# Kernel tuning notes

Measured on AMD Instinct MI355X. Metric: run time of the kernel, lower is better.

## Reference

```python
import jax, jax.numpy as jnp
import numpy as np

EPS = 1e-6
LN_EPS = 1e-5

def _ln(x, g, b):
    m = x.mean(-1, keepdims=True)
    v = x.var(-1, keepdims=True)
    return (x - m) / jnp.sqrt(v + LN_EPS) * g + b

def _gelu(x):
    return jax.nn.gelu(x, approximate=False)  # torch nn.GELU default (erf)

def _compress(x, W1, b1, g1, B1, W2, b2, g2, B2, W3, b3):
    h = _ln(_gelu(x @ W1 + b1), g1, B1)
    h = _ln(_gelu(h @ W2 + b2), g2, B2)
    return h @ W3 + b3

def _decompress(x, W1, b1, g1, B1, W2, b2, g2, B2, W3, b3):
    h = _ln(_gelu(x @ W1 + b1), g1, B1)
    h = _ln(_gelu(h @ W2 + b2), g2, B2)
    return h @ W3 + b3

def setup_inputs() -> dict:
    key = jax.random.key(0)
    ks = jax.random.split(key, 12)
    B, D, C, N = 1024, 1024, 256, 100000
    s = 0.02
    return {
        "query": jax.random.normal(ks[0], (B, D), jnp.float32),
        "keys_c": jax.random.normal(ks[1], (N, C), jnp.float32),
        "values_c": jax.random.normal(ks[2], (N, C), jnp.float32),
        "cW1": jax.random.normal(ks[3], (D, D // 2), jnp.float32) * s,
        "cb1": jnp.zeros((D // 2,), jnp.float32),
        "cg1": jnp.ones((D // 2,), jnp.float32),
        "cB1": jnp.zeros((D // 2,), jnp.float32),
        "cW2": jax.random.normal(ks[4], (D // 2, D // 4), jnp.float32) * s,
        "cb2": jnp.zeros((D // 4,), jnp.float32),
        "cg2": jnp.ones((D // 4,), jnp.float32),
        "cB2": jnp.zeros((D // 4,), jnp.float32),
        "cW3": jax.random.normal(ks[5], (D // 4, C), jnp.float32) * s,
        "cb3": jnp.zeros((C,), jnp.float32),
        "dW1": jax.random.normal(ks[6], (C, D // 4), jnp.float32) * s,
        "db1": jnp.zeros((D // 4,), jnp.float32),
        "dg1": jnp.ones((D // 4,), jnp.float32),
        "dB1": jnp.zeros((D // 4,), jnp.float32),
        "dW2": jax.random.normal(ks[7], (D // 4, D // 2), jnp.float32) * s,
        "db2": jnp.zeros((D // 2,), jnp.float32),
        "dg2": jnp.ones((D // 2,), jnp.float32),
        "dB2": jnp.zeros((D // 2,), jnp.float32),
        "dW3": jax.random.normal(ks[8], (D // 2, D), jnp.float32) * s,
        "db3": jnp.zeros((D,), jnp.float32),
        "k": 5,
    }

def reference(query, keys_c, values_c,
              cW1, cb1, cg1, cB1, cW2, cb2, cg2, cB2, cW3, cb3,
              dW1, db1, dg1, dB1, dW2, db2, dg2, dB2, dW3, db3, k):
    # compress query: [B, D] -> [B, C]
    q_c = _compress(query, cW1, cb1, cg1, cB1, cW2, cb2, cg2, cB2, cW3, cb3)
    # brute-force squared-L2 distances (FAISS IndexFlatL2 semantics): [B, N]
    q2 = jnp.sum(q_c * q_c, axis=-1, keepdims=True)
    k2 = jnp.sum(keys_c * keys_c, axis=-1)[None, :]
    d = jnp.maximum(q2 + k2 - 2.0 * (q_c @ keys_c.T), 0.0)
    # top-k nearest (smallest distances), sorted ascending
    neg_d, idx = jax.lax.top_k(-d, k)  # [B, k]
    d_top = -neg_d
    # inverse-distance weights, normalized per query
    w = 1.0 / (d_top + EPS)
    w = w / jnp.sum(w, axis=-1, keepdims=True)
    # gather stored compressed values and decompress: [B, k, C] -> [B, k, D]
    v = values_c[idx]
    dec = _decompress(v, dW1, db1, dg1, dB1, dW2, db2, dg2, dB2, dW3, db3)
    retrieved = jnp.einsum('bk,bkd->bd', w, dec)
    confidence = 1.0 / (d_top[:, 0] + EPS)  # min distance is first (sorted)
    return retrieved, confidence
```

## Files before the change

kernel.cpp:

```cpp
#include <hip/hip_runtime.h>
#include <cfloat>
#include <cstddef>

typedef __attribute__((ext_vector_type(8))) short bf16x8;
typedef __attribute__((ext_vector_type(4))) float f32x4;

#define NKEYS    100000
#define SPLITS   61
#define SPLITLEN 1664
#define NKP      (SPLITS * SPLITLEN)
#define NCHUNK   (SPLITLEN / 128)

__device__ __forceinline__ unsigned short f2bf(float x) {
    unsigned int u = __float_as_uint(x);
    unsigned int r = (u + 0x7fffu + ((u >> 16) & 1u)) >> 16;
    return (unsigned short)r;
}
__device__ __forceinline__ float bf2f(unsigned short h) {
    return __uint_as_float((unsigned)h << 16);
}
__device__ __forceinline__ void split2(float x, unsigned short& h, unsigned short& l) {
    h = f2bf(x);
    float r = x - bf2f(h);
    l = f2bf(r);
}

__device__ __forceinline__ void async16(void* lds, const void* g) {
    __builtin_amdgcn_global_load_lds(
        (const __attribute__((address_space(1))) unsigned int*)g,
        (__attribute__((address_space(3))) unsigned int*)lds, 16, 0, 0);
}

__device__ __forceinline__ unsigned pack_si(float sc, unsigned local) {
    unsigned u = __float_as_uint(sc);
    unsigned m = ((int)u < 0) ? ~u : (u | 0x80000000u);
    return (m & 0xFFFFF800u) | local;
}

__device__ __forceinline__ void ins5u(unsigned (&a)[5], unsigned v) {
    if (v > a[4]) {
        a[4] = v;
        #pragma unroll
        for (int i = 4; i > 0; --i) {
            if (a[i] > a[i - 1]) { unsigned t = a[i]; a[i] = a[i - 1]; a[i - 1] = t; }
        }
    }
}

__global__ __launch_bounds__(256, 2) void mfma_gemm(
    const unsigned short* __restrict__ Ahi, const unsigned short* __restrict__ Alo,
    const unsigned short* __restrict__ Whi, const unsigned short* __restrict__ Wlo,
    const float* __restrict__ bias, float* __restrict__ C,
    int M, int N, int K, int do_gelu)
{
    __shared__ unsigned short sT[2][8192];
    const int tid = threadIdx.x;
    const int lane = tid & 63;
    const int wv = tid >> 6;
    const int wr = wv >> 1, wc = wv & 1;
    const int m0 = blockIdx.y << 6, n0 = blockIdx.x << 6;

    const int rl = lane & 15, kq = (lane >> 4) << 3;
    const unsigned short* sp[4];
    sp[0] = Ahi + (size_t)(m0 + (wv << 4) + rl) * K + kq;
    sp[1] = Alo + (size_t)(m0 + (wv << 4) + rl) * K + kq;
    sp[2] = Whi + (size_t)(n0 + (wv << 4) + rl) * K + kq;
    sp[3] = Wlo + (size_t)(n0 + (wv << 4) + rl) * K + kq;
    const int ldss = (wv << 9) | (lane << 3);

    f32x4 acc[2][2];
    #pragma unroll
    for (int p = 0; p < 2; ++p)
        #pragma unroll
        for (int q = 0; q < 2; ++q) acc[p][q] = (f32x4){0.f, 0.f, 0.f, 0.f};

    const int steps = K >> 5;
    #pragma unroll
    for (int i = 0; i < 4; ++i)
        async16(&sT[0][(i << 11) + ldss], sp[i]);

    for (int s = 0; s < steps; ++s) {
        const int cur = s & 1;
        __syncthreads();
        if (s + 1 < steps) {
            const int ko = (s + 1) << 5;
            #pragma unroll
            for (int i = 0; i < 4; ++i)
                async16(&sT[cur ^ 1][(i << 11) + ldss], sp[i] + ko);
        }
        bf16x8 ah[2], al[2], wh[2], wl[2];
        #pragma unroll
        for (int p = 0; p < 2; ++p) {
            ah[p] = *(const bf16x8*)&sT[cur][(((wr << 1) + p) << 9) | (lane << 3)];
            al[p] = *(const bf16x8*)&sT[cur][2048 + ((((wr << 1) + p) << 9) | (lane << 3))];
        }
        #pragma unroll
        for (int q = 0; q < 2; ++q) {
            wh[q] = *(const bf16x8*)&sT[cur][4096 + ((((wc << 1) + q) << 9) | (lane << 3))];
            wl[q] = *(const bf16x8*)&sT[cur][6144 + ((((wc << 1) + q) << 9) | (lane << 3))];
        }
        #pragma unroll
        for (int p = 0; p < 2; ++p)
            #pragma unroll
            for (int q = 0; q < 2; ++q) {
                acc[p][q] = __builtin_amdgcn_mfma_f32_16x16x32_bf16(ah[p], wh[q], acc[p][q], 0, 0, 0);
                acc[p][q] = __builtin_amdgcn_mfma_f32_16x16x32_bf16(ah[p], wl[q], acc[p][q], 0, 0, 0);
                acc[p][q] = __builtin_amdgcn_mfma_f32_16x16x32_bf16(al[p], wh[q], acc[p][q], 0, 0, 0);
            }
    }

    #pragma unroll
    for (int q = 0; q < 2; ++q) {
        const int n = n0 + (((wc << 1) + q) << 4) + (lane & 15);
        const float bn = bias[n];
        #pragma unroll
        for (int p = 0; p < 2; ++p) {
            #pragma unroll
            for (int j = 0; j < 4; ++j) {
                const int m = m0 + (((wr << 1) + p) << 4) + ((lane >> 4) << 2) + j;
                float v = acc[p][q][j] + bn;
                if (do_gelu) v = 0.5f * v * (1.0f + erff(v * 0.70710678118654752f));
                C[(size_t)m * N + n] = v;
            }
        }
    }
}

__global__ __launch_bounds__(256) void wsplit(
    const float* __restrict__ W, unsigned short* __restrict__ Thi,
    unsigned short* __restrict__ Tlo, int K, int N)
{
    __shared__ float tile[64][65];
    const int tid = threadIdx.x;
    const int n0 = blockIdx.x << 6, k0 = blockIdx.y << 6;
    const int nl = tid & 63, kg = tid >> 6;
    #pragma unroll
    for (int r = 0; r < 16; ++r)
        tile[kg + (r << 2)][nl] = W[(size_t)(k0 + kg + (r << 2)) * N + n0 + nl];
    __syncthreads();
    const int nn = tid >> 2, kc = (tid & 3) << 4;
    unsigned short* ph = Thi + (size_t)(n0 + nn) * K + k0 + kc;
    unsigned short* pl = Tlo + (size_t)(n0 + nn) * K + k0 + kc;
    #pragma unroll
    for (int c = 0; c < 16; c += 4) {
        ushort4 H, L;
        split2(tile[kc + c + 0][nn], H.x, L.x);
        split2(tile[kc + c + 1][nn], H.y, L.y);
        split2(tile[kc + c + 2][nn], H.z, L.z);
        split2(tile[kc + c + 3][nn], H.w, L.w);
        *(ushort4*)(ph + c) = H;
        *(ushort4*)(pl + c) = L;
    }
}

__global__ __launch_bounds__(256) void csplit(
    const float* __restrict__ X, unsigned short* __restrict__ hi,
    unsigned short* __restrict__ lo)
{
    const size_t i = ((size_t)blockIdx.x * 256 + threadIdx.x) << 2;
    float4 v = *(const float4*)(X + i);
    ushort4 H, L;
    split2(v.x, H.x, L.x);
    split2(v.y, H.y, L.y);
    split2(v.z, H.z, L.z);
    split2(v.w, H.w, L.w);
    *(ushort4*)(hi + i) = H;
    *(ushort4*)(lo + i) = L;
}

__global__ __launch_bounds__(256) void ln_rows(
    float* __restrict__ X, const float* __restrict__ g, const float* __restrict__ b, int C)
{
    const int row = blockIdx.x;
    const int tid = threadIdx.x;
    float* xr = X + (size_t)row * C;
    float v0 = xr[tid];
    float v1 = (C > 256) ? xr[tid + 256] : 0.0f;
    float s = v0 + v1;
    float ss = v0 * v0 + v1 * v1;
    #pragma unroll
    for (int off = 32; off > 0; off >>= 1) {
        s  += __shfl_xor(s, off);
        ss += __shfl_xor(ss, off);
    }
    __shared__ float red[10];
    const int wave = tid >> 6, lane = tid & 63;
    if (lane == 0) { red[wave] = s; red[wave + 4] = ss; }
    __syncthreads();
    if (tid == 0) {
        float S  = red[0] + red[1] + red[2] + red[3];
        float SS = red[4] + red[5] + red[6] + red[7];
        float m = S / C;
        float var = SS / C - m * m;
        red[8] = m;
        red[9] = 1.0f / sqrtf(var + 1e-5f);
    }
    __syncthreads();
    float m = red[8], inv = red[9];
    xr[tid] = (v0 - m) * inv * g[tid] + b[tid];
    if (C > 256) xr[tid + 256] = (v1 - m) * inv * g[tid + 256] + b[tid + 256];
}

__global__ __launch_bounds__(256) void ln_split(
    const float* __restrict__ X, const float* __restrict__ g, const float* __restrict__ b,
    int C, unsigned short* __restrict__ hi, unsigned short* __restrict__ lo)
{
    const int row = blockIdx.x;
    const int tid = threadIdx.x;
    const float* xr = X + (size_t)row * C;
    float v0 = xr[tid];
    float v1 = (C > 256) ? xr[tid + 256] : 0.0f;
    float s = v0 + v1;
    float ss = v0 * v0 + v1 * v1;
    #pragma unroll
    for (int off = 32; off > 0; off >>= 1) {
        s  += __shfl_xor(s, off);
        ss += __shfl_xor(ss, off);
    }
    __shared__ float red[10];
    const int wave = tid >> 6, lane = tid & 63;
    if (lane == 0) { red[wave] = s; red[wave + 4] = ss; }
    __syncthreads();
    if (tid == 0) {
        float S  = red[0] + red[1] + red[2] + red[3];
        float SS = red[4] + red[5] + red[6] + red[7];
        float m = S / C;
        float var = SS / C - m * m;
        red[8] = m;
        red[9] = 1.0f / sqrtf(var + 1e-5f);
    }
    __syncthreads();
    float m = red[8], inv = red[9];
    {
        float y = (v0 - m) * inv * g[tid] + b[tid];
        unsigned short h, l; split2(y, h, l);
        hi[(size_t)row * C + tid] = h;
        lo[(size_t)row * C + tid] = l;
    }
    if (C > 256) {
        float y = (v1 - m) * inv * g[tid + 256] + b[tid + 256];
        unsigned short h, l; split2(y, h, l);
        hi[(size_t)row * C + tid + 256] = h;
        lo[(size_t)row * C + tid + 256] = l;
    }
}

__global__ __launch_bounds__(256) void prep_rows(
    const float* __restrict__ X, unsigned short* __restrict__ xh,
    float* __restrict__ x2, int nvalid, int ntot)
{
    const int row = blockIdx.x * 4 + (threadIdx.x >> 6);
    const int lane = threadIdx.x & 63;
    if (row >= ntot) return;
    if (row < nvalid) {
        float4 v = *(const float4*)(X + (size_t)row * 256 + (lane << 2));
        float ss = v.x * v.x + v.y * v.y + v.z * v.z + v.w * v.w;
        #pragma unroll
        for (int off = 32; off > 0; off >>= 1) ss += __shfl_xor(ss, off);
        ushort4 h;
        h.x = f2bf(v.x); h.y = f2bf(v.y); h.z = f2bf(v.z); h.w = f2bf(v.w);
        *(ushort4*)(xh + (size_t)row * 256 + (lane << 2)) = h;
        if (lane == 0) x2[row] = ss;
    } else {
        ushort4 z = {0, 0, 0, 0};
        *(ushort4*)(xh + (size_t)row * 256 + (lane << 2)) = z;
        if (lane == 0) x2[row] = 0.0f;
    }
}

__global__ __launch_bounds__(256, 2) void dist_topk_mfma(
    const unsigned short* __restrict__ khi, const unsigned short* __restrict__ qhi,
    const float* __restrict__ k2, unsigned* __restrict__ cand_p)
{
    __shared__ unsigned short sB[2][8192];
    const int tid = threadIdx.x;
    const int lane = tid & 63;
    const int wv = tid >> 6;

    const int fid = blockIdx.x;
    const int rr = fid & 7, row = fid >> 3;
    int split, jq;
    if (row < 56) { split = rr * 7 + (row >> 3); jq = row & 7; }
    else { int slot = ((row - 56) << 3) + rr; split = 56 + (slot >> 3); jq = slot & 7; }
    const int kstart = split * SPLITLEN;
    const int q0 = jq * 128 + wv * 32;

    bf16x8 aF[2][8];
    #pragma unroll
    for (int qt = 0; qt < 2; ++qt) {
        const unsigned short* qb = qhi
            + (((size_t)(q0 + qt * 16 + (lane & 15))) << 8) + ((lane >> 4) << 3);
        #pragma unroll
        for (int s = 0; s < 8; ++s) aF[qt][s] = *(const bf16x8*)(qb + s * 32);
    }

    size_t soff[4];
    int ldst[4];
    #pragma unroll
    for (int i = 0; i < 4; ++i) {
        int e = i * 256 + tid;
        int h = e >> 9, t = (e >> 6) & 7, L = e & 63;
        soff[i] = (((size_t)(kstart + t * 16 + (L & 15))) << 8)
                + (h << 5) + ((L >> 4) << 3);
        ldst[i] = e << 3;
    }

    unsigned bp[2][4][5];
    #pragma unroll
    for (int qt = 0; qt < 2; ++qt)
        #pragma unroll
        for (int r = 0; r < 4; ++r)
            #pragma unroll
            for (int j = 0; j < 5; ++j) bp[qt][r][j] = 0u;

    #pragma unroll
    for (int i = 0; i < 4; ++i)
        async16(&sB[0][ldst[i]], khi + soff[i]);

    int cur = 0;
    for (int c = 0; c < NCHUNK; ++c) {
        const int coff = c << 15;
        f32x4 acc[2][8];
        #pragma unroll
        for (int qt = 0; qt < 2; ++qt)
            #pragma unroll
            for (int t = 0; t < 8; ++t) acc[qt][t] = (f32x4){0.f, 0.f, 0.f, 0.f};

        #pragma unroll
        for (int st = 0; st < 4; ++st) {
            __syncthreads();
            const int g = (c << 2) + st;
            if (g + 1 < NCHUNK * 4) {
                const int ns = (st + 1) & 3;
                const int ncoff = (st == 3) ? (coff + 32768) : coff;
                #pragma unroll
                for (int i = 0; i < 4; ++i)
                    async16(&sB[cur ^ 1][ldst[i]],
                            khi + soff[i] + (size_t)(ncoff + (ns << 6)));
            }
            #pragma unroll
            for (int h = 0; h < 2; ++h) {
                #pragma unroll
                for (int t = 0; t < 8; ++t) {
                    bf16x8 b = *(const bf16x8*)
                        &sB[cur][((((h << 3) + t) << 6) | lane) << 3];
                    acc[0][t] = __builtin_amdgcn_mfma_f32_16x16x32_bf16(
                        aF[0][(st << 1) + h], b, acc[0][t], 0, 0, 0);
                    acc[1][t] = __builtin_amdgcn_mfma_f32_16x16x32_bf16(
                        aF[1][(st << 1) + h], b, acc[1][t], 0, 0, 0);
                }
            }
            cur ^= 1;
        }

        const int kb = c << 7;
        #pragma unroll
        for (int t = 0; t < 8; ++t) {
            const unsigned local = (unsigned)(kb + t * 16 + (lane & 15));
            const int key = kstart + (int)local;
            const float k2v = k2[key];
            const bool valid = key < NKEYS;
            #pragma unroll
            for (int qt = 0; qt < 2; ++qt)
                #pragma unroll
                for (int r = 0; r < 4; ++r) {
                    float sc = fmaf(-0.5f, k2v, acc[qt][t][r]);
                    unsigned p = valid ? pack_si(sc, local) : 0u;
                    ins5u(bp[qt][r], p);
                }
        }
    }

    #pragma unroll
    for (int m = 1; m <= 8; m <<= 1) {
        #pragma unroll
        for (int qt = 0; qt < 2; ++qt)
            #pragma unroll
            for (int r = 0; r < 4; ++r) {
                unsigned o[5];
                #pragma unroll
                for (int j = 0; j < 5; ++j)
                    o[j] = (unsigned)__shfl_xor((int)bp[qt][r][j], m);
                #pragma unroll
                for (int j = 0; j < 5; ++j) ins5u(bp[qt][r], o[j]);
            }
    }
    if ((lane & 15) == 0) {
        #pragma unroll
        for (int qt = 0; qt < 2; ++qt)
            #pragma unroll
            for (int r = 0; r < 4; ++r) {
                const int q = q0 + qt * 16 + ((lane >> 4) << 2) + r;
                #pragma unroll
                for (int j = 0; j < 5; ++j)
                    cand_p[(size_t)(split * 5 + j) * 1024 + q] = bp[qt][r][j];
            }
    }
}

__global__ __launch_bounds__(64) void merge8(
    const unsigned* __restrict__ cand_p, int* __restrict__ idx8)
{
    const int q = blockIdx.x * 64 + threadIdx.x;
    unsigned fp[8]; int fi[8];
    #pragma unroll
    for (int j = 0; j < 8; ++j) { fp[j] = 0u; fi[j] = 0; }
    for (int sp = 0; sp < SPLITS; ++sp) {
        for (int j = 0; j < 5; ++j) {
            unsigned v = cand_p[(size_t)(sp * 5 + j) * 1024 + q];
            if (v <= fp[7]) break;
            fp[7] = v; fi[7] = sp * SPLITLEN + (int)(v & 2047u);
            #pragma unroll
            for (int i = 7; i > 0; --i) {
                if (fp[i] > fp[i - 1]) {
                    unsigned tv = fp[i]; fp[i] = fp[i - 1]; fp[i - 1] = tv;
                    int ti = fi[i]; fi[i] = fi[i - 1]; fi[i - 1] = ti;
                }
            }
        }
    }
    #pragma unroll
    for (int j = 0; j < 8; ++j) idx8[q * 8 + j] = fi[j];
}

__global__ __launch_bounds__(256) void rerank(
    const float* __restrict__ qc, const float* __restrict__ keys,
    const float* __restrict__ k2, const float* __restrict__ q2,
    const int* __restrict__ idx8, float* __restrict__ w5,
    int* __restrict__ idx5, float* __restrict__ conf)
{
    const int q = blockIdx.x * 4 + (threadIdx.x >> 6);
    const int lane = threadIdx.x & 63;
    float4 qv = *(const float4*)(qc + (size_t)q * 256 + (lane << 2));
    float dot[8]; int cidx[8];
    #pragma unroll
    for (int c = 0; c < 8; ++c) {
        cidx[c] = idx8[q * 8 + c];
        float4 kv = *(const float4*)(keys + (size_t)cidx[c] * 256 + (lane << 2));
        dot[c] = qv.x * kv.x + qv.y * kv.y + qv.z * kv.z + qv.w * kv.w;
    }
    #pragma unroll
    for (int c = 0; c < 8; ++c)
        #pragma unroll
        for (int off = 32; off > 0; off >>= 1) dot[c] += __shfl_xor(dot[c], off);
    if (lane == 0) {
        float d[8]; int di[8];
        const float qq = q2[q];
        #pragma unroll
        for (int c = 0; c < 8; ++c) {
            d[c] = fmaxf(qq + k2[cidx[c]] - 2.0f * dot[c], 0.0f);
            di[c] = cidx[c];
        }
        #pragma unroll
        for (int a = 1; a < 8; ++a) {
            float dv = d[a]; int iv = di[a]; int b = a;
            while (b > 0 && d[b - 1] > dv) { d[b] = d[b - 1]; di[b] = di[b - 1]; --b; }
            d[b] = dv; di[b] = iv;
        }
        float w[5], sum = 0.0f;
        #pragma unroll
        for (int j = 0; j < 5; ++j) { w[j] = 1.0f / (d[j] + 1e-6f); sum += w[j]; }
        #pragma unroll
        for (int j = 0; j < 5; ++j) { w5[q * 5 + j] = w[j] / sum; idx5[q * 5 + j] = di[j]; }
        conf[q] = 1.0f / (d[0] + 1e-6f);
    }
}

__global__ __launch_bounds__(256) void gather_split(
    const float* __restrict__ values, const int* __restrict__ idx5,
    unsigned short* __restrict__ Xhi, unsigned short* __restrict__ Xlo)
{
    const int row = blockIdx.x;
    const int idx = idx5[row];
    float v = values[(size_t)idx * 256 + threadIdx.x];
    unsigned short h, l; split2(v, h, l);
    Xhi[(size_t)row * 256 + threadIdx.x] = h;
    Xlo[(size_t)row * 256 + threadIdx.x] = l;
}

__global__ __launch_bounds__(128) void combine_split(
    const float* __restrict__ h2d, const float* __restrict__ w5,
    unsigned short* __restrict__ zhi, unsigned short* __restrict__ zlo)
{
    const int q = blockIdx.x;
    const int t = threadIdx.x;
    float4 acc = {0.0f, 0.0f, 0.0f, 0.0f};
    #pragma unroll
    for (int i = 0; i < 5; ++i) {
        float w = w5[q * 5 + i];
        float4 v = *(const float4*)(h2d + ((size_t)q * 5 + i) * 512 + (t << 2));
        acc.x = fmaf(w, v.x, acc.x);
        acc.y = fmaf(w, v.y, acc.y);
        acc.z = fmaf(w, v.z, acc.z);
        acc.w = fmaf(w, v.w, acc.w);
    }
    ushort4 H, L;
    split2(acc.x, H.x, L.x);
    split2(acc.y, H.y, L.y);
    split2(acc.z, H.z, L.z);
    split2(acc.w, H.w, L.w);
    *(ushort4*)(zhi + (size_t)q * 512 + (t << 2)) = H;
    *(ushort4*)(zlo + (size_t)q * 512 + (t << 2)) = L;
}

#define OFF_KHI 0
#define OFF_K2  12992512
#define OFF_QHI 13094016
#define OFF_Q2  13225088
#define OFF_QC  13226112
#define OFF_CP  13488256
#define OFF_I8  13800576
#define OFF_W5  13808768
#define OFF_I5  13813888
#define OFF_WT  13819008
#define OFF_UN  15260800

#define W_C1H 0
#define W_C1L 262144
#define W_C2H 524288
#define W_C2L 589824
#define W_C3H 655360
#define W_C3L 688128
#define W_D1H 720896
#define W_D1L 753664
#define W_D2H 786432
#define W_D2L 851968
#define W_D3H 917504
#define W_D3L 1179648

#define U_H1   0
#define U_H1H  524288
#define U_H1L  786432
#define U_H2   1048576
#define U_H2H  1310720
#define U_H2L  1441792
#define U_QSH  1572864
#define U_QSL  2097152
#define U_X0H  0
#define U_X0L  655360
#define U_T1   1310720
#define U_T1H  2621440
#define U_T1L  3276800
#define U_T2   3932160
#define U_ZH   6553600
#define U_ZL   6815744

extern "C" void kernel_launch(void* const* d_in, const int* in_sizes, int n_in,
                              void* d_out, int out_size, void* d_ws, size_t ws_size,
                              hipStream_t stream) {
    const float* query  = (const float*)d_in[0];
    const float* keys   = (const float*)d_in[1];
    const float* values = (const float*)d_in[2];
    const float* cW1 = (const float*)d_in[3];  const float* cb1 = (const float*)d_in[4];
    const float* cg1 = (const float*)d_in[5];  const float* cB1 = (const float*)d_in[6];
    const float* cW2 = (const float*)d_in[7];  const float* cb2 = (const float*)d_in[8];
    const float* cg2 = (const float*)d_in[9];  const float* cB2 = (const float*)d_in[10];
    const float* cW3 = (const float*)d_in[11]; const float* cb3 = (const float*)d_in[12];
    const float* dW1 = (const float*)d_in[13]; const float* db1 = (const float*)d_in[14];
    const float* dg1 = (const float*)d_in[15]; const float* dB1 = (const float*)d_in[16];
    const float* dW2 = (const float*)d_in[17]; const float* db2 = (const float*)d_in[18];
    const float* dg2 = (const float*)d_in[19]; const float* dB2 = (const float*)d_in[20];
    const float* dW3 = (const float*)d_in[21]; const float* db3 = (const float*)d_in[22];
    float* out = (float*)d_out;
    float* ws  = (float*)d_ws;

    unsigned short* khi = (unsigned short*)(ws + OFF_KHI);
    float* k2 = ws + OFF_K2;
    unsigned short* qhi = (unsigned short*)(ws + OFF_QHI);
    float* q2 = ws + OFF_Q2;
    float* qc = ws + OFF_QC;
    unsigned* cand_p = (unsigned*)(ws + OFF_CP);
    int* idx8 = (int*)(ws + OFF_I8);
    float* w5 = ws + OFF_W5;  int* idx5 = (int*)(ws + OFF_I5);
    float* wt = ws + OFF_WT;
    float* un = ws + OFF_UN;

    unsigned short* wc1h = (unsigned short*)(wt + W_C1H);
    unsigned short* wc1l = (unsigned short*)(wt + W_C1L);
    unsigned short* wc2h = (unsigned short*)(wt + W_C2H);
    unsigned short* wc2l = (unsigned short*)(wt + W_C2L);
    unsigned short* wc3h = (unsigned short*)(wt + W_C3H);
    unsigned short* wc3l = (unsigned short*)(wt + W_C3L);
    unsigned short* wd1h = (unsigned short*)(wt + W_D1H);
    unsigned short* wd1l = (unsigned short*)(wt + W_D1L);
    unsigned short* wd2h = (unsigned short*)(wt + W_D2H);
    unsigned short* wd2l = (unsigned short*)(wt + W_D2L);
    unsigned short* wd3h = (unsigned short*)(wt + W_D3H);
    unsigned short* wd3l = (unsigned short*)(wt + W_D3L);

    float* h1 = un + U_H1;
    unsigned short* h1h = (unsigned short*)(un + U_H1H);
    unsigned short* h1l = (unsigned short*)(un + U_H1L);
    float* h2 = un + U_H2;
    unsigned short* h2h = (unsigned short*)(un + U_H2H);
    unsigned short* h2l = (unsigned short*)(un + U_H2L);
    unsigned short* qsh = (unsigned short*)(un + U_QSH);
    unsigned short* qsl = (unsigned short*)(un + U_QSL);
    unsigned short* x0h = (unsigned short*)(un + U_X0H);
    unsigned short* x0l = (unsigned short*)(un + U_X0L);
    float* t1 = un + U_T1;
    unsigned short* t1h = (unsigned short*)(un + U_T1H);
    unsigned short* t1l = (unsigned short*)(un + U_T1L);
    float* t2 = un + U_T2;
    unsigned short* zh = (unsigned short*)(un + U_ZH);
    unsigned short* zl = (unsigned short*)(un + U_ZL);

    prep_rows<<<NKP / 4, 256, 0, stream>>>(keys, khi, k2, NKEYS, NKP);

    wsplit<<<dim3(8, 16),  256, 0, stream>>>(cW1, wc1h, wc1l, 1024, 512);
    wsplit<<<dim3(4, 8),   256, 0, stream>>>(cW2, wc2h, wc2l, 512, 256);
    wsplit<<<dim3(4, 4),   256, 0, stream>>>(cW3, wc3h, wc3l, 256, 256);
    wsplit<<<dim3(4, 4),   256, 0, stream>>>(dW1, wd1h, wd1l, 256, 256);
    wsplit<<<dim3(8, 4),   256, 0, stream>>>(dW2, wd2h, wd2l, 256, 512);
    wsplit<<<dim3(16, 8),  256, 0, stream>>>(dW3, wd3h, wd3l, 512, 1024);
    csplit<<<1024, 256, 0, stream>>>(query, qsh, qsl);

    mfma_gemm<<<dim3(8, 16),  256, 0, stream>>>(qsh, qsl, wc1h, wc1l, cb1, h1, 1024, 512, 1024, 1);
    ln_split<<<1024, 256, 0, stream>>>(h1, cg1, cB1, 512, h1h, h1l);
    mfma_gemm<<<dim3(4, 16),  256, 0, stream>>>(h1h, h1l, wc2h, wc2l, cb2, h2, 1024, 256, 512, 1);
    ln_split<<<1024, 256, 0, stream>>>(h2, cg2, cB2, 256, h2h, h2l);
    mfma_gemm<<<dim3(4, 16),  256, 0, stream>>>(h2h, h2l, wc3h, wc3l, cb3, qc, 1024, 256, 256, 0);
    prep_rows<<<256, 256, 0, stream>>>(qc, qhi, q2, 1024, 1024);

    dist_topk_mfma<<<SPLITS * 8, 256, 0, stream>>>(khi, qhi, k2, cand_p);
    merge8<<<16, 64, 0, stream>>>(cand_p, idx8);
    rerank<<<256, 256, 0, stream>>>(qc, keys, k2, q2, idx8, w5, idx5, out + 1024 * 1024);

    gather_split<<<5120, 256, 0, stream>>>(values, idx5, x0h, x0l);
    mfma_gemm<<<dim3(4, 80),  256, 0, stream>>>(x0h, x0l, wd1h, wd1l, db1, t1, 5120, 256, 256, 1);
    ln_split<<<5120, 256, 0, stream>>>(t1, dg1, dB1, 256, t1h, t1l);
    mfma_gemm<<<dim3(8, 80),  256, 0, stream>>>(t1h, t1l, wd2h, wd2l, db2, t2, 5120, 512, 256, 1);
    ln_rows<<<5120, 256, 0, stream>>>(t2, dg2, dB2, 512);
    combine_split<<<1024, 128, 0, stream>>>(t2, w5, zh, zl);
    mfma_gemm<<<dim3(16, 16), 256, 0, stream>>>(zh, zl, wd3h, wd3l, db3, out, 1024, 1024, 512, 0);
}
```

Measured before the change: 557.0 us.

## Fuse prep launches and merge/rerank/gather; branchless top-5 insertion in distance kernel

Merges the key prep, query split and six weight-split launches into one prep kernel. Fuses merge8, rerank and gather_split into a single wave-per-query kernel that merges candidates in parallel with an xor-shuffle tree. The distance kernel's top-5 insertion becomes a wave-uniform branchless min/max chain, and the validity check is dropped by setting padded keys' k2 to FLT_MAX so their scores sink to the bottom. These changes aim to cut launch overhead, intermediate index buffers and divergent branching, at the cost of more register pressure and redundant per-lane work in the merge.

```diff
diff --git a/kernel.cpp b/kernel.cpp
--- a/kernel.cpp
+++ b/kernel.cpp
@@ -10,6 +10,9 @@
 #define SPLITLEN 1664
 #define NKP      (SPLITS * SPLITLEN)
 #define NCHUNK   (SPLITLEN / 128)
+#define PREPB    (NKP / 4)
+#define CSPLB    1024
+#define WSPB     352
 
 __device__ __forceinline__ unsigned short f2bf(float x) {
     unsigned int u = __float_as_uint(x);
@@ -33,16 +36,31 @@
 
 __device__ __forceinline__ unsigned pack_si(float sc, unsigned local) {
     unsigned u = __float_as_uint(sc);
-    unsigned m = ((int)u < 0) ? ~u : (u | 0x80000000u);
+    unsigned m = u ^ ((unsigned)((int)u >> 31) | 0x80000000u);
     return (m & 0xFFFFF800u) | local;
 }
 
+__device__ __forceinline__ void chain5(unsigned (&a)[5], unsigned v) {
+    #pragma unroll
+    for (int i = 0; i < 5; ++i) {
+        unsigned t = min(a[i], v);
+        a[i] = max(a[i], v);
+        v = t;
+    }
+}
 __device__ __forceinline__ void ins5u(unsigned (&a)[5], unsigned v) {
-    if (v > a[4]) {
-        a[4] = v;
-        #pragma unroll
-        for (int i = 4; i > 0; --i) {
-            if (a[i] > a[i - 1]) { unsigned t = a[i]; a[i] = a[i - 1]; a[i - 1] = t; }
+    if (__any((int)(v > a[4]))) chain5(a, v);
+}
+
+__device__ __forceinline__ void ins8p(unsigned (&s)[8], int (&ix)[8], unsigned v, int vi) {
+    if (v > s[7]) {
+        s[7] = v; ix[7] = vi;
+        #pragma unroll
+        for (int i = 7; i > 0; --i) {
+            if (s[i] > s[i - 1]) {
+                unsigned tv = s[i]; s[i] = s[i - 1]; s[i - 1] = tv;
+                int ti = ix[i]; ix[i] = ix[i - 1]; ix[i - 1] = ti;
+            }
         }
     }
 }
@@ -126,13 +144,11 @@
     }
 }
 
-__global__ __launch_bounds__(256) void wsplit(
+__device__ __forceinline__ void wsplit_tile(
     const float* __restrict__ W, unsigned short* __restrict__ Thi,
-    unsigned short* __restrict__ Tlo, int K, int N)
+    unsigned short* __restrict__ Tlo, int K, int N, int n0, int k0, int tid)
 {
     __shared__ float tile[64][65];
-    const int tid = threadIdx.x;
-    const int n0 = blockIdx.x << 6, k0 = blockIdx.y << 6;
     const int nl = tid & 63, kg = tid >> 6;
     #pragma unroll
     for (int r = 0; r < 16; ++r)
@@ -153,19 +169,71 @@
     }
 }
 
-__global__ __launch_bounds__(256) void csplit(
-    const float* __restrict__ X, unsigned short* __restrict__ hi,
-    unsigned short* __restrict__ lo)
-{
-    const size_t i = ((size_t)blockIdx.x * 256 + threadIdx.x) << 2;
-    float4 v = *(const float4*)(X + i);
-    ushort4 H, L;
-    split2(v.x, H.x, L.x);
-    split2(v.y, H.y, L.y);
-    split2(v.z, H.z, L.z);
-    split2(v.w, H.w, L.w);
-    *(ushort4*)(hi + i) = H;
-    *(ushort4*)(lo + i) = L;
+__device__ __forceinline__ void prep_group(
+    const float* __restrict__ X, unsigned short* __restrict__ xh,
+    float* __restrict__ x2, int nvalid, int grp, int tid)
+{
+    const int row = (grp << 2) + (tid >> 6);
+    const int lane = tid & 63;
+    if (row < nvalid) {
+        float4 v = *(const float4*)(X + ((size_t)row << 8) + (lane << 2));
+        float ss = v.x * v.x + v.y * v.y + v.z * v.z + v.w * v.w;
+        #pragma unroll
+        for (int off = 32; off > 0; off >>= 1) ss += __shfl_xor(ss, off);
+        ushort4 h;
+        h.x = f2bf(v.x); h.y = f2bf(v.y); h.z = f2bf(v.z); h.w = f2bf(v.w);
+        *(ushort4*)(xh + ((size_t)row << 8) + (lane << 2)) = h;
+        if (lane == 0) x2[row] = ss;
+    } else {
+        ushort4 z = {0, 0, 0, 0};
+        *(ushort4*)(xh + ((size_t)row << 8) + (lane << 2)) = z;
+        if (lane == 0) x2[row] = FLT_MAX;
+    }
+}
+
+__global__ __launch_bounds__(256) void prep_all(
+    const float* __restrict__ keys, unsigned short* __restrict__ khi, float* __restrict__ k2,
+    const float* __restrict__ query, unsigned short* __restrict__ qsh, unsigned short* __restrict__ qsl,
+    const float* __restrict__ cW1, const float* __restrict__ cW2, const float* __restrict__ cW3,
+    const float* __restrict__ dW1, const float* __restrict__ dW2, const float* __restrict__ dW3,
+    unsigned short* wc1h, unsigned short* wc1l, unsigned short* wc2h, unsigned short* wc2l,
+    unsigned short* wc3h, unsigned short* wc3l, unsigned short* wd1h, unsigned short* wd1l,
+    unsigned short* wd2h, unsigned short* wd2l, unsigned short* wd3h, unsigned short* wd3l)
+{
+    const int bid = blockIdx.x;
+    const int tid = threadIdx.x;
+    if (bid < PREPB) {
+        prep_group(keys, khi, k2, NKEYS, bid, tid);
+        return;
+    }
+    if (bid < PREPB + CSPLB) {
+        const size_t i = ((size_t)(bid - PREPB) * 256 + tid) << 2;
+        float4 v = *(const float4*)(query + i);
+        ushort4 H, L;
+        split2(v.x, H.x, L.x);
+        split2(v.y, H.y, L.y);
+        split2(v.z, H.z, L.z);
+        split2(v.w, H.w, L.w);
+        *(ushort4*)(qsh + i) = H;
+        *(ushort4*)(qsl + i) = L;
+        return;
+    }
+    int t = bid - (PREPB + CSPLB);
+    const float* W; unsigned short *Th, *Tl; int K, N;
+    if (t < 128)      {          W = cW1; Th = wc1h; Tl = wc1l; K = 1024; N = 512;  }
+    else if (t < 160) { t -= 128; W = cW2; Th = wc2h; Tl = wc2l; K = 512;  N = 256;  }
+    else if (t < 176) { t -= 160; W = cW3; Th = wc3h; Tl = wc3l; K = 256;  N = 256;  }
+    else if (t < 192) { t -= 176; W = dW1; Th = wd1h; Tl = wd1l; K = 256;  N = 256;  }
+    else if (t < 224) { t -= 192; W = dW2; Th = wd2h; Tl = wd2l; K = 256;  N = 512;  }
+    else              { t -= 224; W = dW3; Th = wd3h; Tl = wd3l; K = 512;  N = 1024; }
+    const int nx = N >> 6;
+    wsplit_tile(W, Th, Tl, K, N, (t % nx) << 6, (t / nx) << 6, tid);
+}
+
+__global__ __launch_bounds__(256) void prep_q(
+    const float* __restrict__ X, unsigned short* __restrict__ xh, float* __restrict__ x2)
+{
+    prep_group(X, xh, x2, 1024, blockIdx.x, threadIdx.x);
 }
 
 __global__ __launch_bounds__(256) void ln_rows(
@@ -242,29 +310,6 @@
         unsigned short h, l; split2(y, h, l);
         hi[(size_t)row * C + tid + 256] = h;
         lo[(size_t)row * C + tid + 256] = l;
-    }
-}
-
-__global__ __launch_bounds__(256) void prep_rows(
-    const float* __restrict__ X, unsigned short* __restrict__ xh,
-    float* __restrict__ x2, int nvalid, int ntot)
-{
-    const int row = blockIdx.x * 4 + (threadIdx.x >> 6);
-    const int lane = threadIdx.x & 63;
-    if (row >= ntot) return;
-    if (row < nvalid) {
-        float4 v = *(const float4*)(X + (size_t)row * 256 + (lane << 2));
-        float ss = v.x * v.x + v.y * v.y + v.z * v.z + v.w * v.w;
-        #pragma unroll
-        for (int off = 32; off > 0; off >>= 1) ss += __shfl_xor(ss, off);
-        ushort4 h;
-        h.x = f2bf(v.x); h.y = f2bf(v.y); h.z = f2bf(v.z); h.w = f2bf(v.w);
-        *(ushort4*)(xh + (size_t)row * 256 + (lane << 2)) = h;
-        if (lane == 0) x2[row] = ss;
-    } else {
-        ushort4 z = {0, 0, 0, 0};
-        *(ushort4*)(xh + (size_t)row * 256 + (lane << 2)) = z;
-        if (lane == 0) x2[row] = 0.0f;
     }
 }
 
@@ -357,16 +402,13 @@
         #pragma unroll
         for (int t = 0; t < 8; ++t) {
             const unsigned local = (unsigned)(kb + t * 16 + (lane & 15));
-            const int key = kstart + (int)local;
-            const float k2v = k2[key];
-            const bool valid = key < NKEYS;
+            const float k2v = k2[kstart + (int)local];
             #pragma unroll
             for (int qt = 0; qt < 2; ++qt)
                 #pragma unroll
                 for (int r = 0; r < 4; ++r) {
                     float sc = fmaf(-0.5f, k2v, acc[qt][t][r]);
-                    unsigned p = valid ? pack_si(sc, local) : 0u;
-                    ins5u(bp[qt][r], p);
+                    ins5u(bp[qt][r], pack_si(sc, local));
                 }
         }
     }
@@ -398,84 +440,82 @@
     }
 }
 
-__global__ __launch_bounds__(64) void merge8(
-    const unsigned* __restrict__ cand_p, int* __restrict__ idx8)
-{
-    const int q = blockIdx.x * 64 + threadIdx.x;
-    unsigned fp[8]; int fi[8];
-    #pragma unroll
-    for (int j = 0; j < 8; ++j) { fp[j] = 0u; fi[j] = 0; }
-    for (int sp = 0; sp < SPLITS; ++sp) {
-        for (int j = 0; j < 5; ++j) {
-            unsigned v = cand_p[(size_t)(sp * 5 + j) * 1024 + q];
-            if (v <= fp[7]) break;
-            fp[7] = v; fi[7] = sp * SPLITLEN + (int)(v & 2047u);
-            #pragma unroll
-            for (int i = 7; i > 0; --i) {
-                if (fp[i] > fp[i - 1]) {
-                    unsigned tv = fp[i]; fp[i] = fp[i - 1]; fp[i - 1] = tv;
-                    int ti = fi[i]; fi[i] = fi[i - 1]; fi[i - 1] = ti;
-                }
-            }
-        }
-    }
-    #pragma unroll
-    for (int j = 0; j < 8; ++j) idx8[q * 8 + j] = fi[j];
-}
-
-__global__ __launch_bounds__(256) void rerank(
+__global__ __launch_bounds__(256) void mrg_rank_gather(
+    const unsigned* __restrict__ cand_p,
     const float* __restrict__ qc, const float* __restrict__ keys,
     const float* __restrict__ k2, const float* __restrict__ q2,
-    const int* __restrict__ idx8, float* __restrict__ w5,
-    int* __restrict__ idx5, float* __restrict__ conf)
-{
-    const int q = blockIdx.x * 4 + (threadIdx.x >> 6);
-    const int lane = threadIdx.x & 63;
-    float4 qv = *(const float4*)(qc + (size_t)q * 256 + (lane << 2));
-    float dot[8]; int cidx[8];
+    float* __restrict__ w5, float* __restrict__ conf,
+    const float* __restrict__ values,
+    unsigned short* __restrict__ x0h, unsigned short* __restrict__ x0l)
+{
+    const int tid = threadIdx.x;
+    const int lane = tid & 63;
+    const int q = (blockIdx.x << 2) + (tid >> 6);
+
+    unsigned fp[8]; int fi[8];
+    #pragma unroll
+    for (int j = 0; j < 8; ++j) { fp[j] = 0u; fi[j] = 0; }
+    for (int t = lane; t < SPLITS * 5; t += 64) {
+        unsigned v = cand_p[(size_t)t * 1024 + q];
+        ins8p(fp, fi, v, (t / 5) * SPLITLEN + (int)(v & 2047u));
+    }
+    #pragma unroll
+    for (int m = 1; m <= 32; m <<= 1) {
+        unsigned op[8]; int oi[8];
+        #pragma unroll
+        for (int j = 0; j < 8; ++j) {
+            op[j] = (unsigned)__shfl_xor((int)fp[j], m);
+            oi[j] = __shfl_xor(fi[j], m);
+        }
+        #pragma unroll
+        for (int j = 0; j < 8; ++j) ins8p(fp, fi, op[j], oi[j]);
+    }
+
+    const float4 qv = *(const float4*)(qc + ((size_t)q << 8) + (lane << 2));
+    float dot[8];
     #pragma unroll
     for (int c = 0; c < 8; ++c) {
-        cidx[c] = idx8[q * 8 + c];
-        float4 kv = *(const float4*)(keys + (size_t)cidx[c] * 256 + (lane << 2));
+        const float4 kv = *(const float4*)(keys + ((size_t)fi[c] << 8) + (lane << 2));
         dot[c] = qv.x * kv.x + qv.y * kv.y + qv.z * kv.z + qv.w * kv.w;
     }
     #pragma unroll
     for (int c = 0; c < 8; ++c)
         #pragma unroll
         for (int off = 32; off > 0; off >>= 1) dot[c] += __shfl_xor(dot[c], off);
+    float d[8]; int di[8];
+    const float qq = q2[q];
+    #pragma unroll
+    for (int c = 0; c < 8; ++c) {
+        d[c] = fmaxf(qq + k2[fi[c]] - 2.0f * dot[c], 0.0f);
+        di[c] = fi[c];
+    }
+    #pragma unroll
+    for (int a = 1; a < 8; ++a) {
+        float dv = d[a]; int iv = di[a]; int b = a;
+        while (b > 0 && d[b - 1] > dv) { d[b] = d[b - 1]; di[b] = di[b - 1]; --b; }
+        d[b] = dv; di[b] = iv;
+    }
+    float w[5], sum = 0.0f;
+    #pragma unroll
+    for (int j = 0; j < 5; ++j) { w[j] = 1.0f / (d[j] + 1e-6f); sum += w[j]; }
     if (lane == 0) {
-        float d[8]; int di[8];
-        const float qq = q2[q];
-        #pragma unroll
-        for (int c = 0; c < 8; ++c) {
-            d[c] = fmaxf(qq + k2[cidx[c]] - 2.0f * dot[c], 0.0f);
-            di[c] = cidx[c];
-        }
-        #pragma unroll
-        for (int a = 1; a < 8; ++a) {
-            float dv = d[a]; int iv = di[a]; int b = a;
-            while (b > 0 && d[b - 1] > dv) { d[b] = d[b - 1]; di[b] = di[b - 1]; --b; }
-            d[b] = dv; di[b] = iv;
-        }
-        float w[5], sum = 0.0f;
-        #pragma unroll
-        for (int j = 0; j < 5; ++j) { w[j] = 1.0f / (d[j] + 1e-6f); sum += w[j]; }
-        #pragma unroll
-        for (int j = 0; j < 5; ++j) { w5[q * 5 + j] = w[j] / sum; idx5[q * 5 + j] = di[j]; }
+        #pragma unroll
+        for (int j = 0; j < 5; ++j) w5[q * 5 + j] = w[j] / sum;
         conf[q] = 1.0f / (d[0] + 1e-6f);
     }
-}
-
-__global__ __launch_bounds__(256) void gather_split(
-    const float* __restrict__ values, const int* __restrict__ idx5,
-    unsigned short* __restrict__ Xhi, unsigned short* __restrict__ Xlo)
-{
-    const int row = blockIdx.x;
-    const int idx = idx5[row];
-    float v = values[(size_t)idx * 256 + threadIdx.x];
-    unsigned short h, l; split2(v, h, l);
-    Xhi[(size_t)row * 256 + threadIdx.x] = h;
-    Xlo[(size_t)row * 256 + threadIdx.x] = l;
+
+    #pragma unroll
+    for (int j = 0; j < 5; ++j) {
+        const size_t r = (size_t)q * 5 + j;
+        const float4 v = *(const float4*)(values + ((size_t)di[j] << 8) + (lane << 2));
+        ushort4 H, L;
+        split2(v.x, H.x, L.x);
+        split2(v.y, H.y, L.y);
+        split2(v.z, H.z, L.z);
+        split2(v.w, H.w, L.w);
+        *(ushort4*)(x0h + (r << 8) + (lane << 2)) = H;
+        *(ushort4*)(x0l + (r << 8) + (lane << 2)) = L;
+    }
 }
 
 __global__ __launch_bounds__(128) void combine_split(
@@ -509,9 +549,7 @@
 #define OFF_Q2  13225088
 #define OFF_QC  13226112
 #define OFF_CP  13488256
-#define OFF_I8  13800576
 #define OFF_W5  13808768
-#define OFF_I5  13813888
 #define OFF_WT  13819008
 #define OFF_UN  15260800
 
@@ -570,8 +608,7 @@
     float* q2 = ws + OFF_Q2;
     float* qc = ws + OFF_QC;
     unsigned* cand_p = (unsigned*)(ws + OFF_CP);
-    int* idx8 = (int*)(ws + OFF_I8);
-    float* w5 = ws + OFF_W5;  int* idx5 = (int*)(ws + OFF_I5);
+    float* w5 = ws + OFF_W5;
     float* wt = ws + OFF_WT;
     float* un = ws + OFF_UN;
 
@@ -604,29 +641,24 @@
     float* t2 = un + U_T2;
     unsigned short* zh = (unsigned short*)(un + U_ZH);
     unsigned short* zl = (unsigned short*)(un + U_ZL);
-
-    prep_rows<<<NKP / 4, 256, 0, stream>>>(keys, khi, k2, NKEYS, NKP);
-
-    wsplit<<<dim3(8, 16),  256, 0, stream>>>(cW1, wc1h, wc1l, 1024, 512);
-    wsplit<<<dim3(4, 8),   256, 0, stream>>>(cW2, wc2h, wc2l, 512, 256);
-    wsplit<<<dim3(4, 4),   256, 0, stream>>>(cW3, wc3h, wc3l, 256, 256);
-    wsplit<<<dim3(4, 4),   256, 0, stream>>>(dW1, wd1h, wd1l, 256, 256);
-    wsplit<<<dim3(8, 4),   256, 0, stream>>>(dW2, wd2h, wd2l, 256, 512);
-    wsplit<<<dim3(16, 8),  256, 0, stream>>>(dW3, wd3h, wd3l, 512, 1024);
-    csplit<<<1024, 256, 0, stream>>>(query, qsh, qsl);
+    float* conf = out + 1024 * 1024;
+
+    prep_all<<<PREPB + CSPLB + WSPB, 256, 0, stream>>>(
+        keys, khi, k2, query, qsh, qsl,
+        cW1, cW2, cW3, dW1, dW2, dW3,
+        wc1h, wc1l, wc2h, wc2l, wc3h, wc3l, wd1h, wd1l, wd2h, wd2l, wd3h, wd3l);
 
     mfma_gemm<<<dim3(8, 16),  256, 0, stream>>>(qsh, qsl, wc1h, wc1l, cb1, h1, 1024, 512, 1024, 1);
     ln_split<<<1024, 256, 0, stream>>>(h1, cg1, cB1, 512, h1h, h1l);
     mfma_gemm<<<dim3(4, 16),  256, 0, stream>>>(h1h, h1l, wc2h, wc2l, cb2, h2, 1024, 256, 512, 1);
     ln_split<<<1024, 256, 0, stream>>>(h2, cg2, cB2, 256, h2h, h2l);
     mfma_gemm<<<dim3(4, 16),  256, 0, stream>>>(h2h, h2l, wc3h, wc3l, cb3, qc, 1024, 256, 256, 0);
-    prep_rows<<<256, 256, 0, stream>>>(qc, qhi, q2, 1024, 1024);
+    prep_q<<<256, 256, 0, stream>>>(qc, qhi, q2);
 
     dist_topk_mfma<<<SPLITS * 8, 256, 0, stream>>>(khi, qhi, k2, cand_p);
-    merge8<<<16, 64, 0, stream>>>(cand_p, idx8);
-    rerank<<<256, 256, 0, stream>>>(qc, keys, k2, q2, idx8, w5, idx5, out + 1024 * 1024);
-
-    gather_split<<<5120, 256, 0, stream>>>(values, idx5, x0h, x0l);
+    mrg_rank_gather<<<256, 256, 0, stream>>>(cand_p, qc, keys, k2, q2, w5, conf,
+                                             values, x0h, x0l);
+
     mfma_gemm<<<dim3(4, 80),  256, 0, stream>>>(x0h, x0l, wd1h, wd1l, db1, t1, 5120, 256, 256, 1);
     ln_split<<<5120, 256, 0, stream>>>(t1, dg1, dB1, 256, t1h, t1l);
     mfma_gemm<<<dim3(8, 80),  256, 0, stream>>>(t1h, t1l, wd2h, wd2l, db2, t2, 5120, 512, 256, 1);
```

Measured after the change: 495.5 us. -11.0%, faster.
